# Kernel optimization log

Measured on AMD Instinct MI355X. Metric: run time of the kernel, lower is better.

Reference implementation:

```python
import jax, jax.numpy as jnp
import numpy as np

KERNEL = 7  # neighborhood window (7x7)
NUM_HEADS = 4


def _window_idx(L, k):
    # NATTEN edge-clamped window start: each query attends to exactly k neighbors.
    starts = jnp.clip(jnp.arange(L) - k // 2, 0, L - k)  # [L]
    return starts[:, None] + jnp.arange(k)[None, :]       # [L, k]


def setup_inputs() -> dict:
    key = jax.random.key(0)
    k1, k2, k3, k4, k5 = jax.random.split(key, 5)
    B, H, W, D = 8, 64, 64, 128
    return {
        "x": jax.random.normal(k1, (B, H, W, D), dtype=jnp.float32),
        "w_qkv": jax.random.normal(k2, (3 * D, D), dtype=jnp.float32) * 0.02,
        "b_qkv": jax.random.normal(k3, (3 * D,), dtype=jnp.float32) * 0.02,
        "w_proj": jax.random.normal(k4, (D, D), dtype=jnp.float32) * 0.02,
        "b_proj": jax.random.normal(k5, (D,), dtype=jnp.float32) * 0.02,
    }


def reference(x, w_qkv, b_qkv, w_proj, b_proj):
    B, H, W, D = x.shape
    nh, k = NUM_HEADS, KERNEL
    hd = D // nh
    scale = hd ** -0.5

    # QKV projection -> [3, B, nh, H, W, hd]
    qkv = x @ w_qkv.T + b_qkv
    qkv = qkv.reshape(B, H, W, 3, nh, hd).transpose(3, 0, 4, 1, 2, 5)
    q, kk, v = qkv[0], qkv[1], qkv[2]

    idx_h = _window_idx(H, k)  # [H, k]
    idx_w = _window_idx(W, k)  # [W, k]
    IH = idx_h[:, None, :, None]  # [H,1,k,1]
    IW = idx_w[None, :, None, :]  # [1,W,1,k]

    # Gather local K/V neighborhoods: [B, nh, H, W, k, k, hd] -> [B, nh, H, W, k*k, hd]
    kn = kk[:, :, IH, IW, :].reshape(B, nh, H, W, k * k, hd)
    vn = v[:, :, IH, IW, :].reshape(B, nh, H, W, k * k, hd)

    attn = jnp.einsum('bhxyd,bhxynd->bhxyn', q * scale, kn)
    attn = jax.nn.softmax(attn, axis=-1)
    out = jnp.einsum('bhxyn,bhxynd->bhxyd', attn, vn)

    out = out.transpose(0, 2, 3, 1, 4).reshape(B, H, W, D)
    return out @ w_proj.T + b_proj
```

## Files before the change

### kernel.cpp

```cpp
#include <hip/hip_runtime.h>
#include <hip/hip_bf16.h>

#define BB 8
#define HH 64
#define WW 64
#define DD 128
#define NH 4
#define HD 32
#define KS 7
#define TS 8
#define HALO 14

typedef __attribute__((ext_vector_type(8))) short short8v;
typedef __attribute__((ext_vector_type(4))) short short4v;
typedef __attribute__((ext_vector_type(4))) float f32x4;
typedef unsigned short bf16_t;

__device__ inline short f2bf(float f) {
  union { float f; unsigned u; } x; x.f = f;
  unsigned r = x.u + 0x7FFFu + ((x.u >> 16) & 1u);
  return (short)(r >> 16);
}

__global__ __launch_bounds__(256) void qkv_mfma(
    const float* __restrict__ x, const float* __restrict__ w,
    const float* __restrict__ bqkv,
    bf16_t* __restrict__ q, bf16_t* __restrict__ k, bf16_t* __restrict__ v) {
  __shared__ __align__(16) short smA[128 * 128];
  __shared__ __align__(16) short smB[128 * 128];
  const int tid = threadIdx.x;
  const int m_tile = blockIdx.x;
  const int n_tile = blockIdx.y;

  const float* Ab = x + (size_t)m_tile * 128 * 128;
  const float* Bb = w + (size_t)n_tile * 128 * 128;
#pragma unroll
  for (int i = 0; i < 8; i++) {
    int idx = tid + i * 256;
    int r = idx >> 4, p = idx & 15;
    const float* ap = Ab + r * 128 + p * 8;
    float4 a0 = *(const float4*)ap;
    float4 a1 = *(const float4*)(ap + 4);
    short8v s;
    s[0] = f2bf(a0.x); s[1] = f2bf(a0.y); s[2] = f2bf(a0.z); s[3] = f2bf(a0.w);
    s[4] = f2bf(a1.x); s[5] = f2bf(a1.y); s[6] = f2bf(a1.z); s[7] = f2bf(a1.w);
    *(short8v*)((char*)smA + ((r * 256 + p * 16) ^ ((r & 7) << 4))) = s;
    const float* bp_ = Bb + r * 128 + p * 8;
    float4 b0 = *(const float4*)bp_;
    float4 b1 = *(const float4*)(bp_ + 4);
    short8v t;
    t[0] = f2bf(b0.x); t[1] = f2bf(b0.y); t[2] = f2bf(b0.z); t[3] = f2bf(b0.w);
    t[4] = f2bf(b1.x); t[5] = f2bf(b1.y); t[6] = f2bf(b1.z); t[7] = f2bf(b1.w);
    *(short8v*)((char*)smB + ((r * 256 + p * 16) ^ ((r & 7) << 4))) = t;
  }
  __syncthreads();

  const int lane = tid & 63;
  const int wid = tid >> 6;
  const int wm = wid >> 1, wn = wid & 1;
  const int l15 = lane & 15, l4 = lane >> 4;

  f32x4 acc[4][4] = {};
  const int rowA0 = wm * 64 + l15;
  const int rowB0 = wn * 64 + l15;
  const int swzA = (rowA0 & 7) << 4;
  const int swzB = (rowB0 & 7) << 4;

#pragma unroll
  for (int ks = 0; ks < 4; ks++) {
    const int cb = ks * 64 + l4 * 16;
    short8v a[4], b[4];
#pragma unroll
    for (int i = 0; i < 4; i++) {
      a[i] = *(const short8v*)((const char*)smA + ((((rowA0 + i * 16) * 256) + cb) ^ swzA));
      b[i] = *(const short8v*)((const char*)smB + ((((rowB0 + i * 16) * 256) + cb) ^ swzB));
    }
#pragma unroll
    for (int mi = 0; mi < 4; mi++)
#pragma unroll
      for (int nj = 0; nj < 4; nj++)
        acc[mi][nj] = __builtin_amdgcn_mfma_f32_16x16x32_bf16(a[mi], b[nj], acc[mi][nj], 0, 0, 0);
  }

  const int bblk = m_tile >> 5;
  const int mrow0 = m_tile * 128 + wm * 64;
  const float qscale = 0.17677669529663687f;
#pragma unroll
  for (int nj = 0; nj < 4; nj++) {
    const int n = n_tile * 128 + wn * 64 + nj * 16 + l15;
    const int which = n >> 7, head = (n >> 5) & 3, d = n & 31;
    bf16_t* outp = (which == 0) ? q : ((which == 1) ? k : v);
    const float bias = bqkv[n];
    const float sc = (which == 0) ? qscale : 1.f;
    bf16_t* obase = outp + ((size_t)(bblk * 4 + head)) * 131072 + d;
#pragma unroll
    for (int mi = 0; mi < 4; mi++) {
#pragma unroll
      for (int r = 0; r < 4; r++) {
        const int m = mrow0 + mi * 16 + l4 * 4 + r;
        const int pix = m & 4095;
        obase[(size_t)pix * 32] = (bf16_t)f2bf((acc[mi][nj][r] + bias) * sc);
      }
    }
  }
}

__global__ __launch_bounds__(256) void attn_mfma(
    const bf16_t* __restrict__ q, const bf16_t* __restrict__ k,
    const bf16_t* __restrict__ v, bf16_t* __restrict__ ao) {
  __shared__ __align__(16) char lds[14336 + 16384];
  char* ksb = lds;
  char* vtb = lds + 14336;

  const int tile = blockIdx.x;
  const int tx = tile >> 3, ty = tile & 7;
  const int head = blockIdx.y, bb = blockIdx.z;
  const size_t bh = ((size_t)bb * NH + head) * 4096;
  const bf16_t* kb = k + bh * HD;
  const bf16_t* vb = v + bh * HD;
  const bf16_t* qb = q + bh * HD;
  const int rstart = min(max(tx * TS - 3, 0), HH - HALO);
  const int cstart = min(max(ty * TS - 3, 0), WW - HALO);
  const int tid = threadIdx.x;
  const int lane = tid & 63, wid = tid >> 6;
  const int l15 = lane & 15, h = lane >> 4;

  short8v qf;
  int qx, qy;
  {
    const int pit = wid * 16 + l15;
    qx = tx * TS + (pit >> 3);
    qy = ty * TS + (pit & 7);
    qf = *(const short8v*)(qb + ((size_t)(qx * WW + qy)) * HD + h * 8);
  }
  const int wx0 = min(max(qx - 3, 0), HH - KS) - rstart;
  const int wy0 = min(max(qy - 3, 0), WW - KS) - cstart;

  for (int idx = tid; idx < 784; idx += 256) {
    const int p = idx >> 2, f = idx & 3;
    const int pr = p / HALO, pc = p % HALO;
    const size_t g = ((size_t)((rstart + pr) * WW + (cstart + pc))) * HD + f * 8;
    short8v kv8 = *(const short8v*)(kb + g);
    const int slot = pr * 16 + pc;
    *(short8v*)(ksb + ((slot * 64 + f * 16) ^ (((slot >> 1) & 3) << 4))) = kv8;
  }
  for (int idx = tid; idx < 784; idx += 256) {
    const int pp = idx >> 3, c = idx & 7;
    const int pr = pp / 7, pc2 = (pp % 7) * 2;
    const size_t g = ((size_t)((rstart + pr) * WW + (cstart + pc2))) * HD + c * 4;
    short4v v0 = *(const short4v*)(vb + g);
    short4v v1 = *(const short4v*)(vb + g + HD);
    const int pos0 = ((pr >> 1) << 5) + ((pc2 >> 2) << 3) + ((pr & 1) << 2) + (pc2 & 3);
#pragma unroll
    for (int j = 0; j < 4; j++) {
      const int d = c * 4 + j;
      const unsigned pk2 = (unsigned)(unsigned short)v0[j] |
                           ((unsigned)(unsigned short)v1[j] << 16);
      *(unsigned*)(vtb + ((d * 512 + pos0 * 2) ^ ((d & 7) << 4))) = pk2;
    }
  }
  for (int idx = tid; idx < 512; idx += 256) {
    const int d = idx >> 4, pr = idx & 15;
    if (pr < 14) {
      const int pos = ((pr >> 1) << 5) + 24 + ((pr & 1) << 2) + 2;
      *(unsigned*)(vtb + ((d * 512 + pos * 2) ^ ((d & 7) << 4))) = 0u;
    }
  }
  __syncthreads();

  f32x4 acc[14];
  const f32x4 zf = {0.f, 0.f, 0.f, 0.f};
  __builtin_amdgcn_s_setprio(1);
#pragma unroll
  for (int nt = 0; nt < 14; nt++) {
    const int slot = nt * 16 + l15;
    short8v kf = *(const short8v*)(ksb + ((slot * 64 + h * 16) ^ (((slot >> 1) & 3) << 4)));
    acc[nt] = __builtin_amdgcn_mfma_f32_16x16x32_bf16(kf, qf, zf, 0, 0, 0);
  }
  __builtin_amdgcn_s_setprio(0);

  bool cv[4];
#pragma unroll
  for (int r = 0; r < 4; r++) cv[r] = ((unsigned)(h * 4 + r - wy0) < 7u);
  float sum = 0.f;
#pragma unroll
  for (int nt = 0; nt < 14; nt++) {
    const bool rv = ((unsigned)(nt - wx0) < 7u);
#pragma unroll
    for (int r = 0; r < 4; r++) {
      const float p = (rv && cv[r]) ? __expf(acc[nt][r]) : 0.f;
      acc[nt][r] = p;
      sum += p;
    }
  }
  sum += __shfl_xor(sum, 16);
  sum += __shfl_xor(sum, 32);
  const float inv = 1.f / sum;

  unsigned pk[14][2];
#pragma unroll
  for (int nt = 0; nt < 14; nt++) {
    pk[nt][0] = (unsigned)(unsigned short)f2bf(acc[nt][0] * inv) |
                ((unsigned)(unsigned short)f2bf(acc[nt][1] * inv) << 16);
    pk[nt][1] = (unsigned)(unsigned short)f2bf(acc[nt][2] * inv) |
                ((unsigned)(unsigned short)f2bf(acc[nt][3] * inv) << 16);
  }

  f32x4 o0 = zf, o1 = zf;
  const int swzv = (l15 & 7) << 4;
  __builtin_amdgcn_s_setprio(1);
#pragma unroll
  for (int kc = 0; kc < 7; kc++) {
    union { unsigned u[4]; short8v s; } pa;
    pa.u[0] = pk[2 * kc][0];     pa.u[1] = pk[2 * kc][1];
    pa.u[2] = pk[2 * kc + 1][0]; pa.u[3] = pk[2 * kc + 1][1];
    const int boff = kc * 64 + h * 16;
    short8v vb0 = *(const short8v*)(vtb + ((l15 * 512 + boff) ^ swzv));
    short8v vb1 = *(const short8v*)(vtb + (((l15 + 16) * 512 + boff) ^ swzv));
    o0 = __builtin_amdgcn_mfma_f32_16x16x32_bf16(pa.s, vb0, o0, 0, 0, 0);
    o1 = __builtin_amdgcn_mfma_f32_16x16x32_bf16(pa.s, vb1, o1, 0, 0, 0);
  }
  __builtin_amdgcn_s_setprio(0);

#pragma unroll
  for (int r = 0; r < 4; r++) {
    const int pit = wid * 16 + h * 4 + r;
    const int x = tx * TS + (pit >> 3), y = ty * TS + (pit & 7);
    bf16_t* op = ao + ((size_t)bb * 4096 + x * WW + y) * DD + head * HD;
    op[l15]      = (bf16_t)f2bf(o0[r]);
    op[l15 + 16] = (bf16_t)f2bf(o1[r]);
  }
}

__global__ __launch_bounds__(256) void proj_mfma(
    const bf16_t* __restrict__ aob, const float* __restrict__ wp,
    const float* __restrict__ bp, float* __restrict__ out) {
  __shared__ __align__(16) short smA[128 * 128];
  __shared__ __align__(16) short smB[128 * 128];
  const int tid = threadIdx.x;
  const int m_tile = blockIdx.x;

  const bf16_t* Ab = aob + (size_t)m_tile * 128 * 128;
#pragma unroll
  for (int i = 0; i < 8; i++) {
    int idx = tid + i * 256;
    int r = idx >> 4, p = idx & 15;
    short8v s = *(const short8v*)(Ab + r * 128 + p * 8);
    *(short8v*)((char*)smA + ((r * 256 + p * 16) ^ ((r & 7) << 4))) = s;
    const float* bp_ = wp + r * 128 + p * 8;
    float4 b0 = *(const float4*)bp_;
    float4 b1 = *(const float4*)(bp_ + 4);
    short8v t;
    t[0] = f2bf(b0.x); t[1] = f2bf(b0.y); t[2] = f2bf(b0.z); t[3] = f2bf(b0.w);
    t[4] = f2bf(b1.x); t[5] = f2bf(b1.y); t[6] = f2bf(b1.z); t[7] = f2bf(b1.w);
    *(short8v*)((char*)smB + ((r * 256 + p * 16) ^ ((r & 7) << 4))) = t;
  }
  __syncthreads();

  const int lane = tid & 63;
  const int wid = tid >> 6;
  const int wm = wid >> 1, wn = wid & 1;
  const int l15 = lane & 15, l4 = lane >> 4;

  f32x4 acc[4][4] = {};
  const int rowA0 = wm * 64 + l15;
  const int rowB0 = wn * 64 + l15;
  const int swzA = (rowA0 & 7) << 4;
  const int swzB = (rowB0 & 7) << 4;

#pragma unroll
  for (int ks = 0; ks < 4; ks++) {
    const int cb = ks * 64 + l4 * 16;
    short8v a[4], b[4];
#pragma unroll
    for (int i = 0; i < 4; i++) {
      a[i] = *(const short8v*)((const char*)smA + ((((rowA0 + i * 16) * 256) + cb) ^ swzA));
      b[i] = *(const short8v*)((const char*)smB + ((((rowB0 + i * 16) * 256) + cb) ^ swzB));
    }
#pragma unroll
    for (int mi = 0; mi < 4; mi++)
#pragma unroll
      for (int nj = 0; nj < 4; nj++)
        acc[mi][nj] = __builtin_amdgcn_mfma_f32_16x16x32_bf16(a[mi], b[nj], acc[mi][nj], 0, 0, 0);
  }

  const int mrow0 = m_tile * 128 + wm * 64;
#pragma unroll
  for (int nj = 0; nj < 4; nj++) {
    const int n = wn * 64 + nj * 16 + l15;
    const float bias = bp[n];
#pragma unroll
    for (int mi = 0; mi < 4; mi++) {
#pragma unroll
      for (int r = 0; r < 4; r++) {
        const int m = mrow0 + mi * 16 + l4 * 4 + r;
        out[(size_t)m * DD + n] = acc[mi][nj][r] + bias;
      }
    }
  }
}

extern "C" void kernel_launch(void* const* d_in, const int* in_sizes, int n_in,
                              void* d_out, int out_size, void* d_ws, size_t ws_size,
                              hipStream_t stream) {
  const float* x      = (const float*)d_in[0];
  const float* w_qkv  = (const float*)d_in[1];
  const float* b_qkv  = (const float*)d_in[2];
  const float* w_proj = (const float*)d_in[3];
  const float* b_proj = (const float*)d_in[4];
  float* out = (float*)d_out;

  const size_t per = (size_t)BB * NH * HH * WW * HD;
  bf16_t* q  = (bf16_t*)d_ws;
  bf16_t* k  = q + per;
  bf16_t* v  = k + per;
  bf16_t* ao = v + per;

  qkv_mfma<<<dim3(256, 3), dim3(256), 0, stream>>>(x, w_qkv, b_qkv, q, k, v);
  attn_mfma<<<dim3(64, NH, BB), dim3(256), 0, stream>>>(q, k, v, ao);
  proj_mfma<<<dim3(256), dim3(256), 0, stream>>>(ao, w_proj, b_proj, out);
}
```

Before: 47.09 us.

## Fuse neighborhood attention with output projection in one kernel per spatial tile

Merges the attention and projection kernels. Each block now handles an 8x8 tile for all four heads in sequence and keeps the bf16 attention output in LDS, then multiplies it by the bf16-converted projection weight loaded once per block. This removes the global write and re-read of the intermediate attention buffer and one kernel launch. In exchange the grid shrinks from 2048 to 512 blocks, heads are processed serially with extra barriers, each block repeats the weight conversion, and LDS use rises to about 62KB, which lowers occupancy.

```diff
diff --git a/kernel.cpp b/kernel.cpp
--- a/kernel.cpp
+++ b/kernel.cpp
@@ -105,196 +105,224 @@
   }
 }
 
-__global__ __launch_bounds__(256) void attn_mfma(
+__device__ __forceinline__ void attn_head(
+    const char* ksb, const char* vtb, const short8v qf,
+    const int l15, const int h4, const int wx0, const bool* cv,
+    unsigned* opk) {
+  f32x4 acc[14];
+  const f32x4 zf = {0.f, 0.f, 0.f, 0.f};
+
+  __builtin_amdgcn_s_setprio(1);
+#pragma unroll
+  for (int nt = 0; nt < 14; nt++) {
+    const int slot = nt * 16 + l15;
+    short8v kf = *(const short8v*)(ksb + ((slot * 64 + h4 * 16) ^ (((slot >> 1) & 3) << 4)));
+    acc[nt] = __builtin_amdgcn_mfma_f32_16x16x32_bf16(kf, qf, zf, 0, 0, 0);
+  }
+  __builtin_amdgcn_s_setprio(0);
+
+  float sum = 0.f;
+#pragma unroll
+  for (int nt = 0; nt < 14; nt++) {
+    const bool rv = ((unsigned)(nt - wx0) < 7u);
+#pragma unroll
+    for (int r = 0; r < 4; r++) {
+      const float p = (rv && cv[r]) ? __expf(acc[nt][r]) : 0.f;
+      acc[nt][r] = p;
+      sum += p;
+    }
+  }
+  sum += __shfl_xor(sum, 16);
+  sum += __shfl_xor(sum, 32);
+  const float inv = 1.f / sum;
+
+  unsigned pk[14][2];
+#pragma unroll
+  for (int nt = 0; nt < 14; nt++) {
+    pk[nt][0] = (unsigned)(unsigned short)f2bf(acc[nt][0] * inv) |
+                ((unsigned)(unsigned short)f2bf(acc[nt][1] * inv) << 16);
+    pk[nt][1] = (unsigned)(unsigned short)f2bf(acc[nt][2] * inv) |
+                ((unsigned)(unsigned short)f2bf(acc[nt][3] * inv) << 16);
+  }
+
+  f32x4 o0 = zf, o1 = zf;
+  const int swzv = (l15 & 7) << 4;
+  __builtin_amdgcn_s_setprio(1);
+#pragma unroll
+  for (int kc = 0; kc < 7; kc++) {
+    union { unsigned u[4]; short8v s; } pa;
+    pa.u[0] = pk[2 * kc][0];     pa.u[1] = pk[2 * kc][1];
+    pa.u[2] = pk[2 * kc + 1][0]; pa.u[3] = pk[2 * kc + 1][1];
+    const int boff = kc * 64 + h4 * 16;
+    short8v vb0 = *(const short8v*)(vtb + ((l15 * 512 + boff) ^ swzv));
+    short8v vb1 = *(const short8v*)(vtb + (((l15 + 16) * 512 + boff) ^ swzv));
+    o0 = __builtin_amdgcn_mfma_f32_16x16x32_bf16(pa.s, vb0, o0, 0, 0, 0);
+    o1 = __builtin_amdgcn_mfma_f32_16x16x32_bf16(pa.s, vb1, o1, 0, 0, 0);
+  }
+  __builtin_amdgcn_s_setprio(0);
+
+  opk[0] = (unsigned)(unsigned short)f2bf(o0[0]) |
+           ((unsigned)(unsigned short)f2bf(o0[1]) << 16);
+  opk[1] = (unsigned)(unsigned short)f2bf(o0[2]) |
+           ((unsigned)(unsigned short)f2bf(o0[3]) << 16);
+  opk[2] = (unsigned)(unsigned short)f2bf(o1[0]) |
+           ((unsigned)(unsigned short)f2bf(o1[1]) << 16);
+  opk[3] = (unsigned)(unsigned short)f2bf(o1[2]) |
+           ((unsigned)(unsigned short)f2bf(o1[3]) << 16);
+}
+
+__global__ __launch_bounds__(256) void attn_proj_fused(
     const bf16_t* __restrict__ q, const bf16_t* __restrict__ k,
-    const bf16_t* __restrict__ v, bf16_t* __restrict__ ao) {
-  __shared__ __align__(16) char lds[14336 + 16384];
-  char* ksb = lds;
-  char* vtb = lds + 14336;
+    const bf16_t* __restrict__ v, const float* __restrict__ wp,
+    const float* __restrict__ bpj, float* __restrict__ out) {
+  __shared__ __align__(16) char lds[63488];
+  char* wpb = lds;
+  char* ksb = lds + 32768;
+  char* vtb = lds + 47104;
+  char* aob = lds + 32768;
 
   const int tile = blockIdx.x;
   const int tx = tile >> 3, ty = tile & 7;
-  const int head = blockIdx.y, bb = blockIdx.z;
-  const size_t bh = ((size_t)bb * NH + head) * 4096;
-  const bf16_t* kb = k + bh * HD;
-  const bf16_t* vb = v + bh * HD;
-  const bf16_t* qb = q + bh * HD;
+  const int bb = blockIdx.y;
   const int rstart = min(max(tx * TS - 3, 0), HH - HALO);
   const int cstart = min(max(ty * TS - 3, 0), WW - HALO);
   const int tid = threadIdx.x;
   const int lane = tid & 63, wid = tid >> 6;
-  const int l15 = lane & 15, h = lane >> 4;
-
-  short8v qf;
+  const int l15 = lane & 15, h4 = lane >> 4;
+
   int qx, qy;
   {
     const int pit = wid * 16 + l15;
     qx = tx * TS + (pit >> 3);
     qy = ty * TS + (pit & 7);
-    qf = *(const short8v*)(qb + ((size_t)(qx * WW + qy)) * HD + h * 8);
-  }
+  }
+  const size_t qoff = (size_t)(qx * WW + qy) * HD + h4 * 8;
+  const size_t bb4 = (size_t)bb * 4;
+  short8v qf0 = *(const short8v*)(q + (bb4 + 0) * 131072 + qoff);
+  short8v qf1 = *(const short8v*)(q + (bb4 + 1) * 131072 + qoff);
+  short8v qf2 = *(const short8v*)(q + (bb4 + 2) * 131072 + qoff);
+  short8v qf3 = *(const short8v*)(q + (bb4 + 3) * 131072 + qoff);
   const int wx0 = min(max(qx - 3, 0), HH - KS) - rstart;
   const int wy0 = min(max(qy - 3, 0), WW - KS) - cstart;
-
-  for (int idx = tid; idx < 784; idx += 256) {
-    const int p = idx >> 2, f = idx & 3;
-    const int pr = p / HALO, pc = p % HALO;
-    const size_t g = ((size_t)((rstart + pr) * WW + (cstart + pc))) * HD + f * 8;
-    short8v kv8 = *(const short8v*)(kb + g);
-    const int slot = pr * 16 + pc;
-    *(short8v*)(ksb + ((slot * 64 + f * 16) ^ (((slot >> 1) & 3) << 4))) = kv8;
-  }
-  for (int idx = tid; idx < 784; idx += 256) {
-    const int pp = idx >> 3, c = idx & 7;
-    const int pr = pp / 7, pc2 = (pp % 7) * 2;
-    const size_t g = ((size_t)((rstart + pr) * WW + (cstart + pc2))) * HD + c * 4;
-    short4v v0 = *(const short4v*)(vb + g);
-    short4v v1 = *(const short4v*)(vb + g + HD);
-    const int pos0 = ((pr >> 1) << 5) + ((pc2 >> 2) << 3) + ((pr & 1) << 2) + (pc2 & 3);
-#pragma unroll
-    for (int j = 0; j < 4; j++) {
-      const int d = c * 4 + j;
-      const unsigned pk2 = (unsigned)(unsigned short)v0[j] |
-                           ((unsigned)(unsigned short)v1[j] << 16);
-      *(unsigned*)(vtb + ((d * 512 + pos0 * 2) ^ ((d & 7) << 4))) = pk2;
-    }
-  }
-  for (int idx = tid; idx < 512; idx += 256) {
-    const int d = idx >> 4, pr = idx & 15;
-    if (pr < 14) {
-      const int pos = ((pr >> 1) << 5) + 24 + ((pr & 1) << 2) + 2;
-      *(unsigned*)(vtb + ((d * 512 + pos * 2) ^ ((d & 7) << 4))) = 0u;
-    }
-  }
-  __syncthreads();
-
-  f32x4 acc[14];
-  const f32x4 zf = {0.f, 0.f, 0.f, 0.f};
-  __builtin_amdgcn_s_setprio(1);
-#pragma unroll
-  for (int nt = 0; nt < 14; nt++) {
-    const int slot = nt * 16 + l15;
-    short8v kf = *(const short8v*)(ksb + ((slot * 64 + h * 16) ^ (((slot >> 1) & 3) << 4)));
-    acc[nt] = __builtin_amdgcn_mfma_f32_16x16x32_bf16(kf, qf, zf, 0, 0, 0);
-  }
-  __builtin_amdgcn_s_setprio(0);
-
   bool cv[4];
 #pragma unroll
-  for (int r = 0; r < 4; r++) cv[r] = ((unsigned)(h * 4 + r - wy0) < 7u);
-  float sum = 0.f;
-#pragma unroll
-  for (int nt = 0; nt < 14; nt++) {
-    const bool rv = ((unsigned)(nt - wx0) < 7u);
-#pragma unroll
-    for (int r = 0; r < 4; r++) {
-      const float p = (rv && cv[r]) ? __expf(acc[nt][r]) : 0.f;
-      acc[nt][r] = p;
-      sum += p;
-    }
-  }
-  sum += __shfl_xor(sum, 16);
-  sum += __shfl_xor(sum, 32);
-  const float inv = 1.f / sum;
-
-  unsigned pk[14][2];
-#pragma unroll
-  for (int nt = 0; nt < 14; nt++) {
-    pk[nt][0] = (unsigned)(unsigned short)f2bf(acc[nt][0] * inv) |
-                ((unsigned)(unsigned short)f2bf(acc[nt][1] * inv) << 16);
-    pk[nt][1] = (unsigned)(unsigned short)f2bf(acc[nt][2] * inv) |
-                ((unsigned)(unsigned short)f2bf(acc[nt][3] * inv) << 16);
-  }
-
-  f32x4 o0 = zf, o1 = zf;
-  const int swzv = (l15 & 7) << 4;
-  __builtin_amdgcn_s_setprio(1);
-#pragma unroll
-  for (int kc = 0; kc < 7; kc++) {
-    union { unsigned u[4]; short8v s; } pa;
-    pa.u[0] = pk[2 * kc][0];     pa.u[1] = pk[2 * kc][1];
-    pa.u[2] = pk[2 * kc + 1][0]; pa.u[3] = pk[2 * kc + 1][1];
-    const int boff = kc * 64 + h * 16;
-    short8v vb0 = *(const short8v*)(vtb + ((l15 * 512 + boff) ^ swzv));
-    short8v vb1 = *(const short8v*)(vtb + (((l15 + 16) * 512 + boff) ^ swzv));
-    o0 = __builtin_amdgcn_mfma_f32_16x16x32_bf16(pa.s, vb0, o0, 0, 0, 0);
-    o1 = __builtin_amdgcn_mfma_f32_16x16x32_bf16(pa.s, vb1, o1, 0, 0, 0);
-  }
-  __builtin_amdgcn_s_setprio(0);
-
-#pragma unroll
-  for (int r = 0; r < 4; r++) {
-    const int pit = wid * 16 + h * 4 + r;
-    const int x = tx * TS + (pit >> 3), y = ty * TS + (pit & 7);
-    bf16_t* op = ao + ((size_t)bb * 4096 + x * WW + y) * DD + head * HD;
-    op[l15]      = (bf16_t)f2bf(o0[r]);
-    op[l15 + 16] = (bf16_t)f2bf(o1[r]);
-  }
-}
-
-__global__ __launch_bounds__(256) void proj_mfma(
-    const bf16_t* __restrict__ aob, const float* __restrict__ wp,
-    const float* __restrict__ bp, float* __restrict__ out) {
-  __shared__ __align__(16) short smA[128 * 128];
-  __shared__ __align__(16) short smB[128 * 128];
-  const int tid = threadIdx.x;
-  const int m_tile = blockIdx.x;
-
-  const bf16_t* Ab = aob + (size_t)m_tile * 128 * 128;
+  for (int r = 0; r < 4; r++) cv[r] = ((unsigned)(h4 * 4 + r - wy0) < 7u);
+
+  auto stage_kv = [&](int hd) {
+    const bf16_t* kb = k + (bb4 + hd) * 131072;
+    const bf16_t* vb = v + (bb4 + hd) * 131072;
+    for (int idx = tid; idx < 784; idx += 256) {
+      const int p = idx >> 2, f = idx & 3;
+      const int pr = p / HALO, pc = p % HALO;
+      const size_t g = ((size_t)((rstart + pr) * WW + (cstart + pc))) * HD + f * 8;
+      short8v kv8 = *(const short8v*)(kb + g);
+      const int slot = pr * 16 + pc;
+      *(short8v*)(ksb + ((slot * 64 + f * 16) ^ (((slot >> 1) & 3) << 4))) = kv8;
+    }
+    for (int idx = tid; idx < 784; idx += 256) {
+      const int pp = idx >> 3, c = idx & 7;
+      const int pr = pp / 7, pc2 = (pp % 7) * 2;
+      const size_t g = ((size_t)((rstart + pr) * WW + (cstart + pc2))) * HD + c * 4;
+      short4v v0 = *(const short4v*)(vb + g);
+      short4v v1 = *(const short4v*)(vb + g + HD);
+      const int pos0 = ((pr >> 1) << 5) + ((pc2 >> 2) << 3) + ((pr & 1) << 2) + (pc2 & 3);
+#pragma unroll
+      for (int j = 0; j < 4; j++) {
+        const int d = c * 4 + j;
+        const unsigned pk2 = (unsigned)(unsigned short)v0[j] |
+                             ((unsigned)(unsigned short)v1[j] << 16);
+        *(unsigned*)(vtb + ((d * 512 + pos0 * 2) ^ ((d & 7) << 4))) = pk2;
+      }
+    }
+  };
+
 #pragma unroll
   for (int i = 0; i < 8; i++) {
     int idx = tid + i * 256;
     int r = idx >> 4, p = idx & 15;
-    short8v s = *(const short8v*)(Ab + r * 128 + p * 8);
-    *(short8v*)((char*)smA + ((r * 256 + p * 16) ^ ((r & 7) << 4))) = s;
     const float* bp_ = wp + r * 128 + p * 8;
     float4 b0 = *(const float4*)bp_;
     float4 b1 = *(const float4*)(bp_ + 4);
     short8v t;
     t[0] = f2bf(b0.x); t[1] = f2bf(b0.y); t[2] = f2bf(b0.z); t[3] = f2bf(b0.w);
     t[4] = f2bf(b1.x); t[5] = f2bf(b1.y); t[6] = f2bf(b1.z); t[7] = f2bf(b1.w);
-    *(short8v*)((char*)smB + ((r * 256 + p * 16) ^ ((r & 7) << 4))) = t;
-  }
-  __syncthreads();
-
-  const int lane = tid & 63;
-  const int wid = tid >> 6;
-  const int wm = wid >> 1, wn = wid & 1;
-  const int l15 = lane & 15, l4 = lane >> 4;
-
-  f32x4 acc[4][4] = {};
-  const int rowA0 = wm * 64 + l15;
-  const int rowB0 = wn * 64 + l15;
-  const int swzA = (rowA0 & 7) << 4;
-  const int swzB = (rowB0 & 7) << 4;
-
+    *(short8v*)(wpb + ((r * 256 + p * 16) ^ ((r & 7) << 4))) = t;
+  }
+  stage_kv(0);
+  for (int idx = tid; idx < 512; idx += 256) {
+    const int d = idx >> 4, pr = idx & 15;
+    if (pr < 14) {
+      const int pos = ((pr >> 1) << 5) + 24 + ((pr & 1) << 2) + 2;
+      *(unsigned*)(vtb + ((d * 512 + pos * 2) ^ ((d & 7) << 4))) = 0u;
+    }
+  }
+  __syncthreads();
+
+  unsigned oph[4][4];
+  attn_head(ksb, vtb, qf0, l15, h4, wx0, cv, oph[0]);
+  __syncthreads();
+  stage_kv(1);
+  __syncthreads();
+  attn_head(ksb, vtb, qf1, l15, h4, wx0, cv, oph[1]);
+  __syncthreads();
+  stage_kv(2);
+  __syncthreads();
+  attn_head(ksb, vtb, qf2, l15, h4, wx0, cv, oph[2]);
+  __syncthreads();
+  stage_kv(3);
+  __syncthreads();
+  attn_head(ksb, vtb, qf3, l15, h4, wx0, cv, oph[3]);
+  __syncthreads();
+
+#pragma unroll
+  for (int hd = 0; hd < 4; hd++) {
+#pragma unroll
+    for (int j = 0; j < 4; j++) {
+      const unsigned u = oph[hd][j];
+      const int row0 = wid * 16 + h4 * 4 + (j & 1) * 2;
+      const int d = hd * 32 + (j >> 1) * 16 + l15;
+      *(bf16_t*)(aob + ((row0 * 256 + d * 2) ^ ((row0 & 7) << 4))) = (bf16_t)(u & 0xFFFFu);
+      const int row1 = row0 + 1;
+      *(bf16_t*)(aob + ((row1 * 256 + d * 2) ^ ((row1 & 7) << 4))) = (bf16_t)(u >> 16);
+    }
+  }
+  __syncthreads();
+
+  f32x4 pacc[4][2] = {};
 #pragma unroll
   for (int ks = 0; ks < 4; ks++) {
-    const int cb = ks * 64 + l4 * 16;
-    short8v a[4], b[4];
-#pragma unroll
-    for (int i = 0; i < 4; i++) {
-      a[i] = *(const short8v*)((const char*)smA + ((((rowA0 + i * 16) * 256) + cb) ^ swzA));
-      b[i] = *(const short8v*)((const char*)smB + ((((rowB0 + i * 16) * 256) + cb) ^ swzB));
-    }
+    const int cb = ks * 64 + h4 * 16;
+    short8v a[4], bfr[2];
+#pragma unroll
+    for (int mi = 0; mi < 4; mi++) {
+      const int row = mi * 16 + l15;
+      a[mi] = *(const short8v*)(aob + ((row * 256 + cb) ^ ((row & 7) << 4)));
+    }
+#pragma unroll
+    for (int t = 0; t < 2; t++) {
+      const int row = (wid * 2 + t) * 16 + l15;
+      bfr[t] = *(const short8v*)(wpb + ((row * 256 + cb) ^ ((row & 7) << 4)));
+    }
+    __builtin_amdgcn_s_setprio(1);
 #pragma unroll
     for (int mi = 0; mi < 4; mi++)
 #pragma unroll
-      for (int nj = 0; nj < 4; nj++)
-        acc[mi][nj] = __builtin_amdgcn_mfma_f32_16x16x32_bf16(a[mi], b[nj], acc[mi][nj], 0, 0, 0);
-  }
-
-  const int mrow0 = m_tile * 128 + wm * 64;
-#pragma unroll
-  for (int nj = 0; nj < 4; nj++) {
-    const int n = wn * 64 + nj * 16 + l15;
-    const float bias = bp[n];
+      for (int t = 0; t < 2; t++)
+        pacc[mi][t] = __builtin_amdgcn_mfma_f32_16x16x32_bf16(a[mi], bfr[t], pacc[mi][t], 0, 0, 0);
+    __builtin_amdgcn_s_setprio(0);
+  }
+
+#pragma unroll
+  for (int t = 0; t < 2; t++) {
+    const int n = (wid * 2 + t) * 16 + l15;
+    const float bias = bpj[n];
 #pragma unroll
     for (int mi = 0; mi < 4; mi++) {
 #pragma unroll
       for (int r = 0; r < 4; r++) {
-        const int m = mrow0 + mi * 16 + l4 * 4 + r;
-        out[(size_t)m * DD + n] = acc[mi][nj][r] + bias;
+        const int pit = mi * 16 + h4 * 4 + r;
+        const int x = tx * TS + (pit >> 3), y = ty * TS + (pit & 7);
+        out[((size_t)bb * 4096 + x * WW + y) * DD + n] = pacc[mi][t][r] + bias;
       }
     }
   }
@@ -311,12 +339,10 @@
   float* out = (float*)d_out;
 
   const size_t per = (size_t)BB * NH * HH * WW * HD;
-  bf16_t* q  = (bf16_t*)d_ws;
-  bf16_t* k  = q + per;
-  bf16_t* v  = k + per;
-  bf16_t* ao = v + per;
+  bf16_t* q = (bf16_t*)d_ws;
+  bf16_t* k = q + per;
+  bf16_t* v = k + per;
 
   qkv_mfma<<<dim3(256, 3), dim3(256), 0, stream>>>(x, w_qkv, b_qkv, q, k, v);
-  attn_mfma<<<dim3(64, NH, BB), dim3(256), 0, stream>>>(q, k, v, ao);
-  proj_mfma<<<dim3(256), dim3(256), 0, stream>>>(ao, w_proj, b_proj, out);
-}
+  attn_proj_fused<<<dim3(64, BB), dim3(256), 0, stream>>>(q, k, v, w_proj, b_proj, out);
+}
```

Measured after the change: 50.76 us. 7.8% more time.

## Stage GEMM epilogues through LDS for vector stores and trim attention row tiles

Applied to the files above, without the earlier changes.

The QKV and projection GEMM epilogues now write their results into shared memory and then issue coalesced 16-byte global stores, replacing scattered 2-byte and 4-byte stores. The attention kernel cuts its QK and PV MFMA loops from 14 to 10 row tiles (7 to 5 K-chunks), starting at a per-wave base row, because each wave's two query rows only need a limited span of halo rows. The cost is extra LDS traffic and barriers in the epilogues, plus base-offset arithmetic in attention that must still cover all valid neighbours.

```diff
diff --git a/kernel.cpp b/kernel.cpp
--- a/kernel.cpp
+++ b/kernel.cpp
@@ -82,26 +82,39 @@
         acc[mi][nj] = __builtin_amdgcn_mfma_f32_16x16x32_bf16(a[mi], b[nj], acc[mi][nj], 0, 0, 0);
   }
 
+  __syncthreads();
+  short* smC = smA;
+  const float qscale = 0.17677669529663687f;
+#pragma unroll
+  for (int nj = 0; nj < 4; nj++) {
+    const int n_local = wn * 64 + nj * 16 + l15;
+    const int n = n_tile * 128 + n_local;
+    const float bias = bqkv[n];
+    const float sc = (n_tile == 0) ? qscale : 1.f;
+#pragma unroll
+    for (int mi = 0; mi < 4; mi++) {
+#pragma unroll
+      for (int r = 0; r < 4; r++) {
+        const int m = wm * 64 + mi * 16 + l4 * 4 + r;
+        *(bf16_t*)((char*)smC + ((m * 256 + n_local * 2) ^ ((m & 7) << 4))) =
+            (bf16_t)f2bf((acc[mi][nj][r] + bias) * sc);
+      }
+    }
+  }
+  __syncthreads();
+
   const int bblk = m_tile >> 5;
-  const int mrow0 = m_tile * 128 + wm * 64;
-  const float qscale = 0.17677669529663687f;
-#pragma unroll
-  for (int nj = 0; nj < 4; nj++) {
-    const int n = n_tile * 128 + wn * 64 + nj * 16 + l15;
-    const int which = n >> 7, head = (n >> 5) & 3, d = n & 31;
-    bf16_t* outp = (which == 0) ? q : ((which == 1) ? k : v);
-    const float bias = bqkv[n];
-    const float sc = (which == 0) ? qscale : 1.f;
-    bf16_t* obase = outp + ((size_t)(bblk * 4 + head)) * 131072 + d;
-#pragma unroll
-    for (int mi = 0; mi < 4; mi++) {
-#pragma unroll
-      for (int r = 0; r < 4; r++) {
-        const int m = mrow0 + mi * 16 + l4 * 4 + r;
-        const int pix = m & 4095;
-        obase[(size_t)pix * 32] = (bf16_t)f2bf((acc[mi][nj][r] + bias) * sc);
-      }
-    }
+  bf16_t* outp = (n_tile == 0) ? q : ((n_tile == 1) ? k : v);
+#pragma unroll
+  for (int i = 0; i < 8; i++) {
+    const int idx = i * 256 + tid;
+    const int h = idx >> 9;
+    const int rem = idx & 511;
+    const int m = rem >> 2, c = rem & 3;
+    short8v t8 = *(const short8v*)((const char*)smC +
+        ((m * 256 + h * 64 + c * 16) ^ ((m & 7) << 4)));
+    const int pix = (m_tile * 128 + m) & 4095;
+    *(short8v*)(outp + ((size_t)(bblk * 4 + h)) * 131072 + (size_t)pix * 32 + c * 8) = t8;
   }
 }
 
@@ -136,6 +149,10 @@
   const int wx0 = min(max(qx - 3, 0), HH - KS) - rstart;
   const int wy0 = min(max(qy - 3, 0), WW - KS) - cstart;
 
+  const int x0 = tx * TS + wid * 2;
+  const int w0 = min(max(x0 - 3, 0), HH - KS) - rstart;
+  const int base = min(w0 & ~1, 4);
+
   for (int idx = tid; idx < 784; idx += 256) {
     const int p = idx >> 2, f = idx & 3;
     const int pr = p / HALO, pc = p % HALO;
@@ -168,12 +185,12 @@
   }
   __syncthreads();
 
-  f32x4 acc[14];
+  f32x4 acc[10];
   const f32x4 zf = {0.f, 0.f, 0.f, 0.f};
   __builtin_amdgcn_s_setprio(1);
 #pragma unroll
-  for (int nt = 0; nt < 14; nt++) {
-    const int slot = nt * 16 + l15;
+  for (int nt = 0; nt < 10; nt++) {
+    const int slot = (base + nt) * 16 + l15;
     short8v kf = *(const short8v*)(ksb + ((slot * 64 + h * 16) ^ (((slot >> 1) & 3) << 4)));
     acc[nt] = __builtin_amdgcn_mfma_f32_16x16x32_bf16(kf, qf, zf, 0, 0, 0);
   }
@@ -184,8 +201,8 @@
   for (int r = 0; r < 4; r++) cv[r] = ((unsigned)(h * 4 + r - wy0) < 7u);
   float sum = 0.f;
 #pragma unroll
-  for (int nt = 0; nt < 14; nt++) {
-    const bool rv = ((unsigned)(nt - wx0) < 7u);
+  for (int nt = 0; nt < 10; nt++) {
+    const bool rv = ((unsigned)(base + nt - wx0) < 7u);
 #pragma unroll
     for (int r = 0; r < 4; r++) {
       const float p = (rv && cv[r]) ? __expf(acc[nt][r]) : 0.f;
@@ -197,9 +214,9 @@
   sum += __shfl_xor(sum, 32);
   const float inv = 1.f / sum;
 
-  unsigned pk[14][2];
-#pragma unroll
-  for (int nt = 0; nt < 14; nt++) {
+  unsigned pk[10][2];
+#pragma unroll
+  for (int nt = 0; nt < 10; nt++) {
     pk[nt][0] = (unsigned)(unsigned short)f2bf(acc[nt][0] * inv) |
                 ((unsigned)(unsigned short)f2bf(acc[nt][1] * inv) << 16);
     pk[nt][1] = (unsigned)(unsigned short)f2bf(acc[nt][2] * inv) |
@@ -208,13 +225,14 @@
 
   f32x4 o0 = zf, o1 = zf;
   const int swzv = (l15 & 7) << 4;
+  const int cbase = (base >> 1) * 64;
   __builtin_amdgcn_s_setprio(1);
 #pragma unroll
-  for (int kc = 0; kc < 7; kc++) {
+  for (int kc = 0; kc < 5; kc++) {
     union { unsigned u[4]; short8v s; } pa;
     pa.u[0] = pk[2 * kc][0];     pa.u[1] = pk[2 * kc][1];
     pa.u[2] = pk[2 * kc + 1][0]; pa.u[3] = pk[2 * kc + 1][1];
-    const int boff = kc * 64 + h * 16;
+    const int boff = cbase + kc * 64 + h * 16;
     short8v vb0 = *(const short8v*)(vtb + ((l15 * 512 + boff) ^ swzv));
     short8v vb1 = *(const short8v*)(vtb + (((l15 + 16) * 512 + boff) ^ swzv));
     o0 = __builtin_amdgcn_mfma_f32_16x16x32_bf16(pa.s, vb0, o0, 0, 0, 0);
@@ -235,8 +253,9 @@
 __global__ __launch_bounds__(256) void proj_mfma(
     const bf16_t* __restrict__ aob, const float* __restrict__ wp,
     const float* __restrict__ bp, float* __restrict__ out) {
-  __shared__ __align__(16) short smA[128 * 128];
-  __shared__ __align__(16) short smB[128 * 128];
+  __shared__ __align__(16) char plds[65536];
+  short* smA = (short*)plds;
+  short* smB = (short*)(plds + 32768);
   const int tid = threadIdx.x;
   const int m_tile = blockIdx.x;
 
@@ -284,7 +303,7 @@
         acc[mi][nj] = __builtin_amdgcn_mfma_f32_16x16x32_bf16(a[mi], b[nj], acc[mi][nj], 0, 0, 0);
   }
 
-  const int mrow0 = m_tile * 128 + wm * 64;
+  __syncthreads();
 #pragma unroll
   for (int nj = 0; nj < 4; nj++) {
     const int n = wn * 64 + nj * 16 + l15;
@@ -293,10 +312,19 @@
     for (int mi = 0; mi < 4; mi++) {
 #pragma unroll
       for (int r = 0; r < 4; r++) {
-        const int m = mrow0 + mi * 16 + l4 * 4 + r;
-        out[(size_t)m * DD + n] = acc[mi][nj][r] + bias;
+        const int m = wm * 64 + mi * 16 + l4 * 4 + r;
+        *(float*)(plds + ((m * 512 + n * 4) ^ ((m & 7) << 5))) = acc[mi][nj][r] + bias;
       }
     }
+  }
+  __syncthreads();
+
+#pragma unroll
+  for (int i = 0; i < 16; i++) {
+    const int idx = i * 256 + tid;
+    const int m = idx >> 5, c = idx & 31;
+    float4 t = *(const float4*)(plds + ((m * 512 + c * 16) ^ ((m & 7) << 5)));
+    *(float4*)(out + (size_t)(m_tile * 128 + m) * DD + c * 4) = t;
   }
 }
 
```

Measured after the change: 46.13 us. 1.02x faster.
